# Performance work log

Hardware: AMD Instinct MI355X
Metric: run time of the kernel (lower is better)

Reference implementation:

```python
import jax, jax.numpy as jnp
import numpy as np

B, N, F, P, HID, OUT = 4, 20000, 8, 12, 64, 1
E = 320000


def _glorot(k, shape):
    lim = float(np.sqrt(6.0 / (shape[0] + shape[1])))
    return jax.random.uniform(k, shape, jnp.float32, -lim, lim)


def setup_inputs() -> dict:
    key = jax.random.key(0)
    ks = jax.random.split(key, 20)
    inp = {
        "x": jax.random.normal(ks[0], (B, N, F, P), jnp.float32),
        "edge_index": jax.random.randint(ks[1], (2, E), 0, N, jnp.int64),
        "edge_attr": jax.random.uniform(ks[2], (E,), jnp.float32),
        # GCNConv weights (stored [in, out]) + biases for z, r, h gates
        "conv_z_w": _glorot(ks[3], (F, HID)), "conv_z_b": jnp.zeros((HID,), jnp.float32),
        "conv_r_w": _glorot(ks[4], (F, HID)), "conv_r_b": jnp.zeros((HID,), jnp.float32),
        "conv_h_w": _glorot(ks[5], (F, HID)), "conv_h_b": jnp.zeros((HID,), jnp.float32),
        # GRU linear layers on cat([conv_out, H]) -> HID (stored [in, out])
        "lin_z_w": _glorot(ks[6], (2 * HID, HID)), "lin_z_b": jnp.zeros((HID,), jnp.float32),
        "lin_r_w": _glorot(ks[7], (2 * HID, HID)), "lin_r_b": jnp.zeros((HID,), jnp.float32),
        "lin_h_w": _glorot(ks[8], (2 * HID, HID)), "lin_h_b": jnp.zeros((HID,), jnp.float32),
        # temporal attention logits over periods
        "attention": jax.random.uniform(ks[9], (P,), jnp.float32),
        # final linear: HID -> OUT*P
        "out_w": _glorot(ks[10], (HID, OUT * P)), "out_b": jnp.zeros((OUT * P,), jnp.float32),
    }
    return inp


def reference(x, edge_index, edge_attr,
              conv_z_w, conv_z_b, conv_r_w, conv_r_b, conv_h_w, conv_h_b,
              lin_z_w, lin_z_b, lin_r_w, lin_r_b, lin_h_w, lin_h_b,
              attention, out_w, out_b):
    Bb, Nn, Ff, Pp = x.shape
    Hh = conv_z_w.shape[1]

    # GCN normalization with self loops: A_hat = D^-1/2 (A + I) D^-1/2
    loop = jnp.arange(Nn)
    row = jnp.concatenate([edge_index[0], loop])
    col = jnp.concatenate([edge_index[1], loop])
    w = jnp.concatenate([edge_attr, jnp.ones((Nn,), x.dtype)])
    deg = jax.ops.segment_sum(w, col, num_segments=Nn)
    dinv = jnp.where(deg > 0, jax.lax.rsqrt(deg), 0.0)
    norm = dinv[row] * w * dinv[col]  # [E+N]

    def gcn(xt, W, b):
        # xt: [B, N, F] -> [B, N, H]
        xw = jnp.einsum('bnf,fh->bnh', xt, W)
        msg = xw[:, row, :] * norm[None, :, None]            # gather over source nodes
        agg = jax.vmap(lambda m: jax.ops.segment_sum(m, col, num_segments=Nn))(msg)
        return agg + b

    H0 = jnp.zeros((Bb, Nn, Hh), x.dtype)  # A3TGCN2 passes H=None each period -> zeros

    def tgcn_cell(xt):
        Z = jax.nn.sigmoid(jnp.concatenate([gcn(xt, conv_z_w, conv_z_b), H0], -1) @ lin_z_w + lin_z_b)
        R = jax.nn.sigmoid(jnp.concatenate([gcn(xt, conv_r_w, conv_r_b), H0], -1) @ lin_r_w + lin_r_b)
        Ht = jnp.tanh(jnp.concatenate([gcn(xt, conv_h_w, conv_h_b), H0 * R], -1) @ lin_h_w + lin_h_b)
        return Z * H0 + (1.0 - Z) * Ht

    probs = jax.nn.softmax(attention)
    xs = jnp.moveaxis(x, -1, 0)  # [P, B, N, F]

    def step(acc, inp):
        xt, p = inp
        return acc + p * tgcn_cell(xt), None

    h_accum, _ = jax.lax.scan(step, jnp.zeros((Bb, Nn, Hh), x.dtype), (xs, probs))

    h = jax.nn.relu(h_accum)
    out = h @ out_w + out_b                 # [B, N, OUT*P]
    return out.reshape(Bb, Nn, -1, Pp)      # [B, N, OUT, P]
```

## Files before the change

### kernel.cpp

```cpp
#include <hip/hip_runtime.h>

#define NN 20000
#define EE 320000
#define CAP 64
#define SVC 72
#define OVCAP 8192

#define WZ_O 0
#define BZ_O 512
#define WH_O 576
#define BH_O 1088
#define OWT_O 1152
#define OB_O 1968
#define PR_O 1980
#define NCONST 1992

__device__ __forceinline__ float b2f(unsigned short h) {
  union { unsigned int u; float f; } v; v.u = ((unsigned int)h) << 16; return v.f;
}
__device__ __forceinline__ unsigned short f2b(float f) {
  union { unsigned int u; float f; } v; v.f = f;
  unsigned int u = v.u;
  unsigned int r = (u + 0x7fffu + ((u >> 16) & 1u)) >> 16;
  return (unsigned short)r;
}
__device__ __forceinline__ float ldw(const void* p, int i, int isbf) {
  return isbf ? b2f(((const unsigned short*)p)[i]) : ((const float*)p)[i];
}
__device__ __forceinline__ void upk(unsigned int w, float& x0, float& x1) {
  union { unsigned int u; float f; } lo, hi;
  lo.u = w << 16; hi.u = w & 0xffff0000u;
  x0 = lo.f; x1 = hi.f;
}
__device__ __forceinline__ float degf(unsigned long long dc) {
  return (float)(unsigned int)dc * (1.0f / 1048576.0f);
}

__global__ void k_init(const unsigned int* __restrict__ ei_w,
                       const unsigned int* __restrict__ ea_w,
                       int* __restrict__ flags,
                       unsigned long long* __restrict__ degcnt,
                       int* __restrict__ ovf_cnt,
                       float* __restrict__ consts,
                       const void* czw, const void* czb,
                       const void* chw, const void* chb,
                       const void* lzw, const void* lzb,
                       const void* lhw, const void* lhb,
                       const void* att, const void* ow, const void* ob) {
  int tid = threadIdx.x;
  int i = blockIdx.x * 256 + tid;
  if (i < NN) degcnt[i] = 0ull;
  if (blockIdx.x == 1 && tid == 0) *ovf_cnt = 0;
  if (blockIdx.x != 0) return;

  __shared__ int sfl[2];
  if (tid < 64) {
    unsigned long long b1 = __ballot((ea_w[tid] >> 15) & 1u);
    unsigned long long b2 = __ballot(ei_w[2 * tid + 1] != 0u);
    if (tid == 0) {
      int f0 = (b1 == 0ull) ? 1 : 0;
      int f1 = (b2 == 0ull) ? 1 : 0;
      flags[0] = f0; flags[1] = f1; sfl[0] = f0; sfl[1] = f1;
    }
  }
  __syncthreads();
  int isbf = sfl[0];

  for (int idx = tid; idx < 512; idx += 256) {
    int f = idx >> 6, k = idx & 63;
    float sz = 0.f, sh = 0.f;
    for (int h = 0; h < 64; ++h) {
      sz += ldw(czw, f * 64 + h, isbf) * ldw(lzw, h * 64 + k, isbf);
      sh += ldw(chw, f * 64 + h, isbf) * ldw(lhw, h * 64 + k, isbf);
    }
    consts[WZ_O + idx] = sz; consts[WH_O + idx] = sh;
  }
  for (int idx = tid; idx < 64; idx += 256) {
    float sz = ldw(lzb, idx, isbf), sh = ldw(lhb, idx, isbf);
    for (int h = 0; h < 64; ++h) {
      sz += ldw(czb, h, isbf) * ldw(lzw, h * 64 + idx, isbf);
      sh += ldw(chb, h, isbf) * ldw(lhw, h * 64 + idx, isbf);
    }
    consts[BZ_O + idx] = sz; consts[BH_O + idx] = sh;
  }
  for (int idx = tid; idx < 816; idx += 256) {
    int p = idx / 68, kk = idx % 68;
    consts[OWT_O + idx] = (kk < 64) ? ldw(ow, kk * 12 + p, isbf) : 0.f;
  }
  if (tid < 12) consts[OB_O + tid] = ldw(ob, tid, isbf);
  if (tid == 0) {
    float a[12]; float m = -1e30f;
    for (int p = 0; p < 12; ++p) { a[p] = ldw(att, p, isbf); m = fmaxf(m, a[p]); }
    float ssum = 0.f;
    for (int p = 0; p < 12; ++p) { a[p] = __expf(a[p] - m); ssum += a[p]; }
    for (int p = 0; p < 12; ++p) consts[PR_O + p] = a[p] / ssum;
  }
}

__global__ void k_append(const void* __restrict__ ei, const void* __restrict__ ea,
                         const int* __restrict__ flags,
                         unsigned long long* __restrict__ degcnt,
                         unsigned int* __restrict__ slab,
                         int* __restrict__ ovf_cnt, int* __restrict__ ovf_dst,
                         unsigned int* __restrict__ ovf_pack) {
  int isbf = flags[0], is64 = flags[1];
  int e = blockIdx.x * blockDim.x + threadIdx.x;
  if (e >= EE) return;
  int r, c;
  if (is64) {
    r = (int)((const unsigned int*)ei)[2 * e];
    c = (int)((const unsigned int*)ei)[2 * (EE + e)];
  } else {
    r = ((const int*)ei)[e];
    c = ((const int*)ei)[EE + e];
  }
  unsigned short wb;
  float w;
  if (isbf) { wb = ((const unsigned short*)ea)[e]; w = b2f(wb); }
  else      { w = ((const float*)ea)[e]; wb = f2b(w); }
  unsigned long long pk = (1ull << 32) |
      (unsigned long long)(unsigned int)__float2int_rn(w * 1048576.0f);
  unsigned long long old = atomicAdd(&degcnt[c], pk);
  int pos = (int)(old >> 32);
  unsigned int packed = ((unsigned int)wb << 16) | (unsigned int)r;
  if (pos < CAP) {
    slab[c * CAP + pos] = packed;
  } else {
    int oi = atomicAdd(ovf_cnt, 1);
    if (oi < OVCAP) { ovf_dst[oi] = c; ovf_pack[oi] = packed; }
  }
}

#define ACC8(u, v)                                           \
  { float x0, x1;                                            \
    upk((u).x, x0, x1); a[0] += (v) * x0; a[1] += (v) * x1;  \
    upk((u).y, x0, x1); a[2] += (v) * x0; a[3] += (v) * x1;  \
    upk((u).z, x0, x1); a[4] += (v) * x0; a[5] += (v) * x1;  \
    upk((u).w, x0, x1); a[6] += (v) * x0; a[7] += (v) * x1; }

#define ACCF8(u0, u1, v)                                                       \
  { a[0] += (v) * (u0).x; a[1] += (v) * (u0).y; a[2] += (v) * (u0).z;          \
    a[3] += (v) * (u0).w; a[4] += (v) * (u1).x; a[5] += (v) * (u1).y;          \
    a[6] += (v) * (u1).z; a[7] += (v) * (u1).w; }

__global__ void __launch_bounds__(256) k_node(
    const void* __restrict__ x,
    const unsigned long long* __restrict__ degcnt,
    const unsigned int* __restrict__ slab,
    const int* __restrict__ ovf_cnt, const int* __restrict__ ovf_dst,
    const unsigned int* __restrict__ ovf_pack,
    const float* __restrict__ consts, const int* __restrict__ flags,
    void* __restrict__ out) {
  __shared__ __align__(16) float sow[840];
  __shared__ __align__(16) int2  sv[4 * SVC];
  __shared__ __align__(16) float accT[4 * 384];
  __shared__ __align__(16) float hw[4 * 272];
  __shared__ int swcnt[4];

  const int tid  = threadIdx.x;
  const int w    = tid >> 6;
  const int lane = tid & 63;
  const int isbf = flags[0];
  const int n    = blockIdx.x * 4 + w;

  for (int i = tid; i < 840; i += 256) sow[i] = consts[OWT_O + i];
  float wz[8], wh[8];
#pragma unroll
  for (int f = 0; f < 8; ++f) {
    wz[f] = consts[WZ_O + f * 64 + lane];
    wh[f] = consts[WH_O + f * 64 + lane];
  }
  const float bz = consts[BZ_O + lane], bh = consts[BH_O + lane];

  unsigned long long dcn = degcnt[n];
  int cnt = (int)(dcn >> 32);
  int base = cnt < CAP ? cnt : CAP;
  const float dn = rsqrtf(degf(dcn) + 1.0f);
  int2* svw = &sv[w * SVC];
  if (lane == 0) swcnt[w] = base;
  if (lane < base) {
    unsigned int pk = slab[n * CAP + lane];
    int s = (int)(pk & 0xffffu);
    float v = b2f((unsigned short)(pk >> 16)) * rsqrtf(degf(degcnt[s]) + 1.0f);
    svw[lane] = make_int2(s * 96, __float_as_int(v));
  }
  int m0 = base;
  {
    int ov = ovf_cnt[0];
    if (ov > 0) {
      if (ov > OVCAP) ov = OVCAP;
      for (int i = lane; i < ov; i += 64) {
        if (ovf_dst[i] == n) {
          int idx = atomicAdd(&swcnt[w], 1);
          if (idx < SVC - 1) {
            unsigned int pk = ovf_pack[i];
            int s = (int)(pk & 0xffffu);
            float v = b2f((unsigned short)(pk >> 16)) * rsqrtf(degf(degcnt[s]) + 1.0f);
            svw[idx] = make_int2(s * 96, __float_as_int(v));
          }
        }
      }
      __builtin_amdgcn_wave_barrier();
      m0 = swcnt[w];
      if (m0 > SVC - 1) m0 = SVC - 1;
    }
  }
  if (lane == 0) svw[m0] = make_int2(n * 96, __float_as_int(dn));
  const int m1 = m0 + 1;
  __syncthreads();

  float a[8];
#pragma unroll
  for (int t = 0; t < 8; ++t) a[t] = 0.f;
  if (lane < 48) {
    const long xbase = (long)(lane / 12) * (NN * 96) + 8 * (lane % 12);
    if (isbf) {
      const unsigned short* xb = (const unsigned short*)x;
      int j = 0;
      for (; j + 1 < m1; j += 2) {
        int2 e0 = svw[j], e1 = svw[j + 1];
        uint4 u0 = *(const uint4*)(xb + xbase + e0.x);
        uint4 u1 = *(const uint4*)(xb + xbase + e1.x);
        float v0 = __int_as_float(e0.y), v1 = __int_as_float(e1.y);
        ACC8(u0, v0); ACC8(u1, v1);
      }
      if (j < m1) {
        int2 e0 = svw[j];
        uint4 u0 = *(const uint4*)(xb + xbase + e0.x);
        float v0 = __int_as_float(e0.y);
        ACC8(u0, v0);
      }
    } else {
      const float* xf = (const float*)x;
      int j = 0;
      for (; j + 1 < m1; j += 2) {
        int2 e0 = svw[j], e1 = svw[j + 1];
        const float4* p0 = (const float4*)(xf + xbase + e0.x);
        const float4* p1 = (const float4*)(xf + xbase + e1.x);
        float4 u00 = p0[0], u01 = p0[1], u10 = p1[0], u11 = p1[1];
        float v0 = __int_as_float(e0.y), v1 = __int_as_float(e1.y);
        ACCF8(u00, u01, v0); ACCF8(u10, u11, v1);
      }
      if (j < m1) {
        int2 e0 = svw[j];
        const float4* p0 = (const float4*)(xf + xbase + e0.x);
        float4 u00 = p0[0], u01 = p0[1];
        float v0 = __int_as_float(e0.y);
        ACCF8(u00, u01, v0);
      }
    }
    float* accTw = &accT[w * 384];
    const int bq = (lane / 12) * 96, oc = 8 * (lane % 12);
#pragma unroll
    for (int t = 0; t < 8; ++t) {
      int eib = oc + t;
      int f = eib / 12, p = eib % 12;
      accTw[bq + p * 8 + f] = dn * a[t];
    }
  }
  __builtin_amdgcn_wave_barrier();

  {
    const float* accTw = &accT[w * 384];
    float* hww = &hw[w * 272];
#pragma unroll
    for (int b = 0; b < 4; ++b) {
      float hbl = 0.f;
#pragma unroll
      for (int p = 0; p < 12; ++p) {
        const float4* A = (const float4*)&accTw[b * 96 + p * 8];
        float4 A0 = A[0], A1 = A[1];
        float za = bz + A0.x * wz[0] + A0.y * wz[1] + A0.z * wz[2] + A0.w * wz[3]
                      + A1.x * wz[4] + A1.y * wz[5] + A1.z * wz[6] + A1.w * wz[7];
        float ta = bh + A0.x * wh[0] + A0.y * wh[1] + A0.z * wh[2] + A0.w * wh[3]
                      + A1.x * wh[4] + A1.y * wh[5] + A1.z * wh[6] + A1.w * wh[7];
        float ea = __expf(za);
        float eh = __expf(2.0f * fminf(ta, 40.0f));
        hbl += sow[828 + p] * (eh - 1.0f) *
               __builtin_amdgcn_rcpf((1.0f + ea) * (1.0f + eh));
      }
      hww[b * 68 + lane] = fmaxf(hbl, 0.f);
    }
  }
  __builtin_amdgcn_wave_barrier();

  if (lane < 48) {
    const float* hww = &hw[w * 272];
    int b = lane / 12, p = lane % 12;
    float o = sow[816 + p];
#pragma unroll
    for (int kq = 0; kq < 16; ++kq) {
      float4 hv = *(const float4*)&hww[b * 68 + 4 * kq];
      float4 wv = *(const float4*)&sow[p * 68 + 4 * kq];
      o += hv.x * wv.x + hv.y * wv.y + hv.z * wv.z + hv.w * wv.w;
    }
    int oi = (b * NN + n) * 12 + p;
    if (isbf) ((unsigned short*)out)[oi] = f2b(o);
    else      ((float*)out)[oi] = o;
  }
}

extern "C" void kernel_launch(void* const* d_in, const int* in_sizes, int n_in,
                              void* d_out, int out_size, void* d_ws, size_t ws_size,
                              hipStream_t stream) {
  const void* x   = d_in[0];
  const void* ei  = d_in[1];
  const void* ea  = d_in[2];
  const void* czw = d_in[3];
  const void* czb = d_in[4];
  const void* chw = d_in[7];
  const void* chb = d_in[8];
  const void* lzw = d_in[9];
  const void* lzb = d_in[10];
  const void* lhw = d_in[13];
  const void* lhb = d_in[14];
  const void* att = d_in[15];
  const void* ow  = d_in[16];
  const void* ob  = d_in[17];

  char* ws = (char*)d_ws;
  int*   flags   = (int*)  (ws + 0);
  float* consts  = (float*)(ws + 256);
  unsigned long long* degcnt = (unsigned long long*)(ws + 8448);
  int*   ovf_cnt = (int*)  (ws + 168448);
  int*   ovf_dst = (int*)  (ws + 168704);
  unsigned int* ovf_pack = (unsigned int*)(ws + 201472);
  unsigned int* slab     = (unsigned int*)(ws + 240000);

  k_init<<<dim3(79), dim3(256), 0, stream>>>((const unsigned int*)ei,
                                             (const unsigned int*)ea, flags, degcnt,
                                             ovf_cnt, consts, czw, czb, chw, chb,
                                             lzw, lzb, lhw, lhb, att, ow, ob);
  k_append<<<dim3(1250), dim3(256), 0, stream>>>(ei, ea, flags, degcnt, slab,
                                                 ovf_cnt, ovf_dst, ovf_pack);
  k_node<<<dim3(NN / 4), dim3(256), 0, stream>>>(x, degcnt, slab, ovf_cnt, ovf_dst,
                                                 ovf_pack, consts, flags, d_out);
}
```

Baseline: 240.4 us.

## Pad degree counters to separate cache lines and use all 64 lanes for gather

The per-node degree/count atomics are spaced 8 entries (64 bytes) apart so that concurrent atomics from different edges do not contend on the same cache line. Downstream workspace offsets are moved to make room. The gather loop in the node kernel now spreads each node's 384 feature elements over all 64 lanes at 6 elements each, instead of 48 lanes at 8, so no lanes sit idle. In exchange, the loads become 12-byte and 24-byte accesses instead of 16-byte vectors, and the padded degree array spreads the degree reads over more cache lines.

Result: slower. 245.9 us (+2.3%).

```diff
diff --git a/kernel.cpp b/kernel.cpp
--- a/kernel.cpp
+++ b/kernel.cpp
@@ -5,6 +5,7 @@
 #define CAP 64
 #define SVC 72
 #define OVCAP 8192
+#define DSTR 8
 
 #define WZ_O 0
 #define BZ_O 512
@@ -35,6 +36,9 @@
 __device__ __forceinline__ float degf(unsigned long long dc) {
   return (float)(unsigned int)dc * (1.0f / 1048576.0f);
 }
+
+struct __attribute__((aligned(4))) U3 { unsigned int x, y, z; };
+struct __attribute__((aligned(8))) F6 { float f0,f1,f2,f3,f4,f5; };
 
 __global__ void k_init(const unsigned int* __restrict__ ei_w,
                        const unsigned int* __restrict__ ea_w,
@@ -49,7 +53,7 @@
                        const void* att, const void* ow, const void* ob) {
   int tid = threadIdx.x;
   int i = blockIdx.x * 256 + tid;
-  if (i < NN) degcnt[i] = 0ull;
+  if (i < NN) degcnt[i * DSTR] = 0ull;
   if (blockIdx.x == 1 && tid == 0) *ovf_cnt = 0;
   if (blockIdx.x != 0) return;
 
@@ -120,7 +124,7 @@
   else      { w = ((const float*)ea)[e]; wb = f2b(w); }
   unsigned long long pk = (1ull << 32) |
       (unsigned long long)(unsigned int)__float2int_rn(w * 1048576.0f);
-  unsigned long long old = atomicAdd(&degcnt[c], pk);
+  unsigned long long old = atomicAdd(&degcnt[c * DSTR], pk);
   int pos = (int)(old >> 32);
   unsigned int packed = ((unsigned int)wb << 16) | (unsigned int)r;
   if (pos < CAP) {
@@ -131,17 +135,15 @@
   }
 }
 
-#define ACC8(u, v)                                           \
+#define ACC6(u, v)                                           \
   { float x0, x1;                                            \
     upk((u).x, x0, x1); a[0] += (v) * x0; a[1] += (v) * x1;  \
     upk((u).y, x0, x1); a[2] += (v) * x0; a[3] += (v) * x1;  \
-    upk((u).z, x0, x1); a[4] += (v) * x0; a[5] += (v) * x1;  \
-    upk((u).w, x0, x1); a[6] += (v) * x0; a[7] += (v) * x1; }
-
-#define ACCF8(u0, u1, v)                                                       \
-  { a[0] += (v) * (u0).x; a[1] += (v) * (u0).y; a[2] += (v) * (u0).z;          \
-    a[3] += (v) * (u0).w; a[4] += (v) * (u1).x; a[5] += (v) * (u1).y;          \
-    a[6] += (v) * (u1).z; a[7] += (v) * (u1).w; }
+    upk((u).z, x0, x1); a[4] += (v) * x0; a[5] += (v) * x1; }
+
+#define ACCF6(u, v)                                                     \
+  { a[0] += (v) * (u).f0; a[1] += (v) * (u).f1; a[2] += (v) * (u).f2;   \
+    a[3] += (v) * (u).f3; a[4] += (v) * (u).f4; a[5] += (v) * (u).f5; }
 
 __global__ void __launch_bounds__(256) k_node(
     const void* __restrict__ x,
@@ -172,7 +174,7 @@
   }
   const float bz = consts[BZ_O + lane], bh = consts[BH_O + lane];
 
-  unsigned long long dcn = degcnt[n];
+  unsigned long long dcn = degcnt[n * DSTR];
   int cnt = (int)(dcn >> 32);
   int base = cnt < CAP ? cnt : CAP;
   const float dn = rsqrtf(degf(dcn) + 1.0f);
@@ -181,7 +183,7 @@
   if (lane < base) {
     unsigned int pk = slab[n * CAP + lane];
     int s = (int)(pk & 0xffffu);
-    float v = b2f((unsigned short)(pk >> 16)) * rsqrtf(degf(degcnt[s]) + 1.0f);
+    float v = b2f((unsigned short)(pk >> 16)) * rsqrtf(degf(degcnt[s * DSTR]) + 1.0f);
     svw[lane] = make_int2(s * 96, __float_as_int(v));
   }
   int m0 = base;
@@ -195,7 +197,8 @@
           if (idx < SVC - 1) {
             unsigned int pk = ovf_pack[i];
             int s = (int)(pk & 0xffffu);
-            float v = b2f((unsigned short)(pk >> 16)) * rsqrtf(degf(degcnt[s]) + 1.0f);
+            float v = b2f((unsigned short)(pk >> 16)) *
+                      rsqrtf(degf(degcnt[s * DSTR]) + 1.0f);
             svw[idx] = make_int2(s * 96, __float_as_int(v));
           }
         }
@@ -209,53 +212,50 @@
   const int m1 = m0 + 1;
   __syncthreads();
 
-  float a[8];
-#pragma unroll
-  for (int t = 0; t < 8; ++t) a[t] = 0.f;
-  if (lane < 48) {
-    const long xbase = (long)(lane / 12) * (NN * 96) + 8 * (lane % 12);
+  float a[6];
+#pragma unroll
+  for (int t = 0; t < 6; ++t) a[t] = 0.f;
+  {
+    const long xbase = (long)(lane >> 4) * (NN * 96) + 6 * (lane & 15);
     if (isbf) {
       const unsigned short* xb = (const unsigned short*)x;
       int j = 0;
       for (; j + 1 < m1; j += 2) {
         int2 e0 = svw[j], e1 = svw[j + 1];
-        uint4 u0 = *(const uint4*)(xb + xbase + e0.x);
-        uint4 u1 = *(const uint4*)(xb + xbase + e1.x);
+        U3 u0 = *(const U3*)(xb + xbase + e0.x);
+        U3 u1 = *(const U3*)(xb + xbase + e1.x);
         float v0 = __int_as_float(e0.y), v1 = __int_as_float(e1.y);
-        ACC8(u0, v0); ACC8(u1, v1);
+        ACC6(u0, v0); ACC6(u1, v1);
       }
       if (j < m1) {
         int2 e0 = svw[j];
-        uint4 u0 = *(const uint4*)(xb + xbase + e0.x);
+        U3 u0 = *(const U3*)(xb + xbase + e0.x);
         float v0 = __int_as_float(e0.y);
-        ACC8(u0, v0);
+        ACC6(u0, v0);
       }
     } else {
       const float* xf = (const float*)x;
       int j = 0;
       for (; j + 1 < m1; j += 2) {
         int2 e0 = svw[j], e1 = svw[j + 1];
-        const float4* p0 = (const float4*)(xf + xbase + e0.x);
-        const float4* p1 = (const float4*)(xf + xbase + e1.x);
-        float4 u00 = p0[0], u01 = p0[1], u10 = p1[0], u11 = p1[1];
+        F6 u0 = *(const F6*)(xf + xbase + e0.x);
+        F6 u1 = *(const F6*)(xf + xbase + e1.x);
         float v0 = __int_as_float(e0.y), v1 = __int_as_float(e1.y);
-        ACCF8(u00, u01, v0); ACCF8(u10, u11, v1);
+        ACCF6(u0, v0); ACCF6(u1, v1);
       }
       if (j < m1) {
         int2 e0 = svw[j];
-        const float4* p0 = (const float4*)(xf + xbase + e0.x);
-        float4 u00 = p0[0], u01 = p0[1];
+        F6 u0 = *(const F6*)(xf + xbase + e0.x);
         float v0 = __int_as_float(e0.y);
-        ACCF8(u00, u01, v0);
+        ACCF6(u0, v0);
       }
     }
     float* accTw = &accT[w * 384];
-    const int bq = (lane / 12) * 96, oc = 8 * (lane % 12);
-#pragma unroll
-    for (int t = 0; t < 8; ++t) {
-      int eib = oc + t;
-      int f = eib / 12, p = eib % 12;
-      accTw[bq + p * 8 + f] = dn * a[t];
+#pragma unroll
+    for (int t = 0; t < 6; ++t) {
+      int e = 6 * lane + t;
+      int b = e / 96, r = e % 96, f = r / 12, p = r % 12;
+      accTw[b * 96 + p * 8 + f] = dn * a[t];
     }
   }
   __builtin_amdgcn_wave_barrier();
@@ -322,10 +322,10 @@
   int*   flags   = (int*)  (ws + 0);
   float* consts  = (float*)(ws + 256);
   unsigned long long* degcnt = (unsigned long long*)(ws + 8448);
-  int*   ovf_cnt = (int*)  (ws + 168448);
-  int*   ovf_dst = (int*)  (ws + 168704);
-  unsigned int* ovf_pack = (unsigned int*)(ws + 201472);
-  unsigned int* slab     = (unsigned int*)(ws + 240000);
+  int*   ovf_cnt = (int*)  (ws + 1288448);
+  int*   ovf_dst = (int*)  (ws + 1288704);
+  unsigned int* ovf_pack = (unsigned int*)(ws + 1321472);
+  unsigned int* slab     = (unsigned int*)(ws + 1354240);
 
   k_init<<<dim3(79), dim3(256), 0, stream>>>((const unsigned int*)ei,
                                              (const unsigned int*)ea, flags, degcnt,
```

## Fuse init into append kernel, pad degree counters, zero via memset

Applied to the files above, without the earlier changes.

Merges the constant-folding init kernel into the edge-append kernel as an extra block and lets each append block process four edges per thread. Degree/count atomics are padded to a stride of 8 entries (64 bytes) so different nodes' counters fall in different cache lines, which is meant to reduce atomic contention. The workspace is zeroed with a single memset instead of by the init kernel. Padding enlarges the degree array eightfold and makes the node kernel's gathered degree reads sparser, and the memset adds a separate operation on the stream.

Result: faster. 233.4 us (-2.9%).

```diff
diff --git a/kernel.cpp b/kernel.cpp
--- a/kernel.cpp
+++ b/kernel.cpp
@@ -5,6 +5,8 @@
 #define CAP 64
 #define SVC 72
 #define OVCAP 8192
+#define DSTR 8
+#define EBLK 313
 
 #define WZ_O 0
 #define BZ_O 512
@@ -36,98 +38,91 @@
   return (float)(unsigned int)dc * (1.0f / 1048576.0f);
 }
 
-__global__ void k_init(const unsigned int* __restrict__ ei_w,
-                       const unsigned int* __restrict__ ea_w,
-                       int* __restrict__ flags,
-                       unsigned long long* __restrict__ degcnt,
-                       int* __restrict__ ovf_cnt,
-                       float* __restrict__ consts,
-                       const void* czw, const void* czb,
-                       const void* chw, const void* chb,
-                       const void* lzw, const void* lzb,
-                       const void* lhw, const void* lhb,
-                       const void* att, const void* ow, const void* ob) {
-  int tid = threadIdx.x;
-  int i = blockIdx.x * 256 + tid;
-  if (i < NN) degcnt[i] = 0ull;
-  if (blockIdx.x == 1 && tid == 0) *ovf_cnt = 0;
-  if (blockIdx.x != 0) return;
-
+__global__ void __launch_bounds__(256) k_append(
+    const void* __restrict__ ei, const void* __restrict__ ea,
+    unsigned long long* __restrict__ degcnt,
+    unsigned int* __restrict__ slab,
+    int* __restrict__ ovf_cnt, int* __restrict__ ovf_dst,
+    unsigned int* __restrict__ ovf_pack,
+    int* __restrict__ flags, float* __restrict__ consts,
+    const void* czw, const void* czb, const void* chw, const void* chb,
+    const void* lzw, const void* lzb, const void* lhw, const void* lhb,
+    const void* att, const void* ow, const void* ob) {
   __shared__ int sfl[2];
+  const int tid = threadIdx.x;
   if (tid < 64) {
-    unsigned long long b1 = __ballot((ea_w[tid] >> 15) & 1u);
-    unsigned long long b2 = __ballot(ei_w[2 * tid + 1] != 0u);
+    unsigned long long b1 = __ballot((((const unsigned int*)ea)[tid] >> 15) & 1u);
+    unsigned long long b2 = __ballot(((const unsigned int*)ei)[2 * tid + 1] != 0u);
     if (tid == 0) {
-      int f0 = (b1 == 0ull) ? 1 : 0;
-      int f1 = (b2 == 0ull) ? 1 : 0;
-      flags[0] = f0; flags[1] = f1; sfl[0] = f0; sfl[1] = f1;
+      sfl[0] = (b1 == 0ull) ? 1 : 0;
+      sfl[1] = (b2 == 0ull) ? 1 : 0;
     }
   }
   __syncthreads();
-  int isbf = sfl[0];
-
-  for (int idx = tid; idx < 512; idx += 256) {
-    int f = idx >> 6, k = idx & 63;
-    float sz = 0.f, sh = 0.f;
-    for (int h = 0; h < 64; ++h) {
-      sz += ldw(czw, f * 64 + h, isbf) * ldw(lzw, h * 64 + k, isbf);
-      sh += ldw(chw, f * 64 + h, isbf) * ldw(lhw, h * 64 + k, isbf);
-    }
-    consts[WZ_O + idx] = sz; consts[WH_O + idx] = sh;
-  }
-  for (int idx = tid; idx < 64; idx += 256) {
-    float sz = ldw(lzb, idx, isbf), sh = ldw(lhb, idx, isbf);
-    for (int h = 0; h < 64; ++h) {
-      sz += ldw(czb, h, isbf) * ldw(lzw, h * 64 + idx, isbf);
-      sh += ldw(chb, h, isbf) * ldw(lhw, h * 64 + idx, isbf);
-    }
-    consts[BZ_O + idx] = sz; consts[BH_O + idx] = sh;
-  }
-  for (int idx = tid; idx < 816; idx += 256) {
-    int p = idx / 68, kk = idx % 68;
-    consts[OWT_O + idx] = (kk < 64) ? ldw(ow, kk * 12 + p, isbf) : 0.f;
-  }
-  if (tid < 12) consts[OB_O + tid] = ldw(ob, tid, isbf);
-  if (tid == 0) {
-    float a[12]; float m = -1e30f;
-    for (int p = 0; p < 12; ++p) { a[p] = ldw(att, p, isbf); m = fmaxf(m, a[p]); }
-    float ssum = 0.f;
-    for (int p = 0; p < 12; ++p) { a[p] = __expf(a[p] - m); ssum += a[p]; }
-    for (int p = 0; p < 12; ++p) consts[PR_O + p] = a[p] / ssum;
-  }
-}
-
-__global__ void k_append(const void* __restrict__ ei, const void* __restrict__ ea,
-                         const int* __restrict__ flags,
-                         unsigned long long* __restrict__ degcnt,
-                         unsigned int* __restrict__ slab,
-                         int* __restrict__ ovf_cnt, int* __restrict__ ovf_dst,
-                         unsigned int* __restrict__ ovf_pack) {
-  int isbf = flags[0], is64 = flags[1];
-  int e = blockIdx.x * blockDim.x + threadIdx.x;
-  if (e >= EE) return;
-  int r, c;
-  if (is64) {
-    r = (int)((const unsigned int*)ei)[2 * e];
-    c = (int)((const unsigned int*)ei)[2 * (EE + e)];
-  } else {
-    r = ((const int*)ei)[e];
-    c = ((const int*)ei)[EE + e];
-  }
-  unsigned short wb;
-  float w;
-  if (isbf) { wb = ((const unsigned short*)ea)[e]; w = b2f(wb); }
-  else      { w = ((const float*)ea)[e]; wb = f2b(w); }
-  unsigned long long pk = (1ull << 32) |
-      (unsigned long long)(unsigned int)__float2int_rn(w * 1048576.0f);
-  unsigned long long old = atomicAdd(&degcnt[c], pk);
-  int pos = (int)(old >> 32);
-  unsigned int packed = ((unsigned int)wb << 16) | (unsigned int)r;
-  if (pos < CAP) {
-    slab[c * CAP + pos] = packed;
-  } else {
-    int oi = atomicAdd(ovf_cnt, 1);
-    if (oi < OVCAP) { ovf_dst[oi] = c; ovf_pack[oi] = packed; }
+  const int isbf = sfl[0], is64 = sfl[1];
+
+  if (blockIdx.x == EBLK) {
+    if (tid == 0) { flags[0] = isbf; flags[1] = is64; }
+    for (int idx = tid; idx < 512; idx += 256) {
+      int f = idx >> 6, k = idx & 63;
+      float sz = 0.f, sh = 0.f;
+      for (int h = 0; h < 64; ++h) {
+        sz += ldw(czw, f * 64 + h, isbf) * ldw(lzw, h * 64 + k, isbf);
+        sh += ldw(chw, f * 64 + h, isbf) * ldw(lhw, h * 64 + k, isbf);
+      }
+      consts[WZ_O + idx] = sz; consts[WH_O + idx] = sh;
+    }
+    for (int idx = tid; idx < 64; idx += 256) {
+      float sz = ldw(lzb, idx, isbf), sh = ldw(lhb, idx, isbf);
+      for (int h = 0; h < 64; ++h) {
+        sz += ldw(czb, h, isbf) * ldw(lzw, h * 64 + idx, isbf);
+        sh += ldw(chb, h, isbf) * ldw(lhw, h * 64 + idx, isbf);
+      }
+      consts[BZ_O + idx] = sz; consts[BH_O + idx] = sh;
+    }
+    for (int idx = tid; idx < 816; idx += 256) {
+      int p = idx / 68, kk = idx % 68;
+      consts[OWT_O + idx] = (kk < 64) ? ldw(ow, kk * 12 + p, isbf) : 0.f;
+    }
+    if (tid < 12) consts[OB_O + tid] = ldw(ob, tid, isbf);
+    if (tid == 0) {
+      float a[12]; float m = -1e30f;
+      for (int p = 0; p < 12; ++p) { a[p] = ldw(att, p, isbf); m = fmaxf(m, a[p]); }
+      float ssum = 0.f;
+      for (int p = 0; p < 12; ++p) { a[p] = __expf(a[p] - m); ssum += a[p]; }
+      for (int p = 0; p < 12; ++p) consts[PR_O + p] = a[p] / ssum;
+    }
+    return;
+  }
+
+  const int e0 = blockIdx.x * 1024 + tid;
+#pragma unroll
+  for (int u = 0; u < 4; ++u) {
+    int e = e0 + 256 * u;
+    if (e >= EE) continue;
+    int r, c;
+    if (is64) {
+      r = (int)((const unsigned int*)ei)[2 * e];
+      c = (int)((const unsigned int*)ei)[2 * (EE + e)];
+    } else {
+      r = ((const int*)ei)[e];
+      c = ((const int*)ei)[EE + e];
+    }
+    unsigned short wb;
+    float w;
+    if (isbf) { wb = ((const unsigned short*)ea)[e]; w = b2f(wb); }
+    else      { w = ((const float*)ea)[e]; wb = f2b(w); }
+    unsigned long long pk = (1ull << 32) |
+        (unsigned long long)(unsigned int)__float2int_rn(w * 1048576.0f);
+    unsigned long long old = atomicAdd(&degcnt[c * DSTR], pk);
+    int pos = (int)(old >> 32);
+    unsigned int packed = ((unsigned int)wb << 16) | (unsigned int)r;
+    if (pos < CAP) {
+      slab[c * CAP + pos] = packed;
+    } else {
+      int oi = atomicAdd(ovf_cnt, 1);
+      if (oi < OVCAP) { ovf_dst[oi] = c; ovf_pack[oi] = packed; }
+    }
   }
 }
 
@@ -172,7 +167,7 @@
   }
   const float bz = consts[BZ_O + lane], bh = consts[BH_O + lane];
 
-  unsigned long long dcn = degcnt[n];
+  unsigned long long dcn = degcnt[n * DSTR];
   int cnt = (int)(dcn >> 32);
   int base = cnt < CAP ? cnt : CAP;
   const float dn = rsqrtf(degf(dcn) + 1.0f);
@@ -181,7 +176,7 @@
   if (lane < base) {
     unsigned int pk = slab[n * CAP + lane];
     int s = (int)(pk & 0xffffu);
-    float v = b2f((unsigned short)(pk >> 16)) * rsqrtf(degf(degcnt[s]) + 1.0f);
+    float v = b2f((unsigned short)(pk >> 16)) * rsqrtf(degf(degcnt[s * DSTR]) + 1.0f);
     svw[lane] = make_int2(s * 96, __float_as_int(v));
   }
   int m0 = base;
@@ -195,7 +190,8 @@
           if (idx < SVC - 1) {
             unsigned int pk = ovf_pack[i];
             int s = (int)(pk & 0xffffu);
-            float v = b2f((unsigned short)(pk >> 16)) * rsqrtf(degf(degcnt[s]) + 1.0f);
+            float v = b2f((unsigned short)(pk >> 16)) *
+                      rsqrtf(degf(degcnt[s * DSTR]) + 1.0f);
             svw[idx] = make_int2(s * 96, __float_as_int(v));
           }
         }
@@ -321,18 +317,19 @@
   char* ws = (char*)d_ws;
   int*   flags   = (int*)  (ws + 0);
   float* consts  = (float*)(ws + 256);
-  unsigned long long* degcnt = (unsigned long long*)(ws + 8448);
-  int*   ovf_cnt = (int*)  (ws + 168448);
-  int*   ovf_dst = (int*)  (ws + 168704);
-  unsigned int* ovf_pack = (unsigned int*)(ws + 201472);
-  unsigned int* slab     = (unsigned int*)(ws + 240000);
-
-  k_init<<<dim3(79), dim3(256), 0, stream>>>((const unsigned int*)ei,
-                                             (const unsigned int*)ea, flags, degcnt,
-                                             ovf_cnt, consts, czw, czb, chw, chb,
-                                             lzw, lzb, lhw, lhb, att, ow, ob);
-  k_append<<<dim3(1250), dim3(256), 0, stream>>>(ei, ea, flags, degcnt, slab,
-                                                 ovf_cnt, ovf_dst, ovf_pack);
+  unsigned long long* degcnt = (unsigned long long*)(ws + 8704);
+  int*   ovf_cnt = (int*)  (ws + 1288704);
+  int*   ovf_dst = (int*)  (ws + 1288768);
+  unsigned int* ovf_pack = (unsigned int*)(ws + 1321536);
+  unsigned int* slab     = (unsigned int*)(ws + 1354304);
+
+  hipMemsetAsync(ws + 8704, 0, 1280064, stream);
+  k_append<<<dim3(EBLK + 1), dim3(256), 0, stream>>>(ei, ea, degcnt, slab,
+                                                     ovf_cnt, ovf_dst, ovf_pack,
+                                                     flags, consts,
+                                                     czw, czb, chw, chb,
+                                                     lzw, lzb, lhw, lhb,
+                                                     att, ow, ob);
   k_node<<<dim3(NN / 4), dim3(256), 0, stream>>>(x, degcnt, slab, ovf_cnt, ovf_dst,
                                                  ovf_pack, consts, flags, d_out);
 }
```
